# Kernel optimization log

Measured on AMD Instinct MI355X. Metric: run time of the kernel, lower is better.

Reference implementation:

```python
import jax, jax.numpy as jnp
import numpy as np

NEG_SLOPE = 0.2  # GATConv attention leaky_relu slope (init arg)
POST_SLOPE = 0.2  # leaky_relu after LayerNorm in outer forward
N_LAYERS = 3


def _leaky(x, slope):
    return jnp.where(x >= 0, x, slope * x)


def _layer_norm(x, g, b):
    mu = jnp.mean(x, axis=-1, keepdims=True)
    var = jnp.var(x, axis=-1, keepdims=True)
    return (x - mu) * jax.lax.rsqrt(var + 1e-5) * g + b


def _gat_conv(h, W, al, ar, bias, src, dst, apply_act):
    # DGL GATConv (eval mode, dropout = identity)
    N = h.shape[0]
    H, D = al.shape
    feat = (h @ W).reshape(N, H, D)                      # [N,H,D]
    el = jnp.einsum('nhd,hd->nh', feat, al)              # [N,H]
    er = jnp.einsum('nhd,hd->nh', feat, ar)              # [N,H]
    e = _leaky(el[src] + er[dst], NEG_SLOPE)             # [E,H] edge logits
    # segment (per-destination) softmax, numerically stable
    m = jax.ops.segment_max(e, dst, num_segments=N)      # [N,H]
    ex = jnp.exp(e - m[dst])                             # [E,H]
    s = jax.ops.segment_sum(ex, dst, num_segments=N)     # [N,H]
    alpha = ex / s[dst]                                  # [E,H]
    msg = alpha[:, :, None] * feat[src]                  # [E,H,D]
    rst = jax.ops.segment_sum(msg, dst, num_segments=N)  # [N,H,D]
    rst = rst + bias.reshape(1, H, D)
    if apply_act:
        rst = jax.nn.elu(rst)
    return rst


def setup_inputs() -> dict:
    key = jax.random.key(0)
    ks = jax.random.split(key, 12)
    N, E, IN, D, H, C = 100000, 1600000, 256, 64, 4, 40
    HID = H * D  # 256
    sc = 0.05
    return {
        'x': jax.random.normal(ks[0], (N, IN), jnp.float32),
        'W_h': jax.random.normal(ks[1], (3, IN, HID), jnp.float32) * sc,
        'attn_l_h': jax.random.normal(ks[2], (3, H, D), jnp.float32) * sc,
        'attn_r_h': jax.random.normal(ks[3], (3, H, D), jnp.float32) * sc,
        'bias_h': jnp.zeros((3, HID), jnp.float32),
        'ln_g': jnp.ones((3, HID), jnp.float32),
        'ln_b': jnp.zeros((3, HID), jnp.float32),
        'W_o': jax.random.normal(ks[4], (HID, C), jnp.float32) * sc,
        'attn_l_o': jax.random.normal(ks[5], (1, C), jnp.float32) * sc,
        'attn_r_o': jax.random.normal(ks[6], (1, C), jnp.float32) * sc,
        'bias_o': jnp.zeros((C,), jnp.float32),
        'edge_src': jax.random.randint(ks[7], (E,), 0, N, jnp.int32),
        'edge_dst': jax.random.randint(ks[8], (E,), 0, N, jnp.int32),
    }


def reference(x, W_h, attn_l_h, attn_r_h, bias_h, ln_g, ln_b,
              W_o, attn_l_o, attn_r_o, bias_o, edge_src, edge_dst):
    h = x
    for l in range(N_LAYERS):
        hn = _gat_conv(h, W_h[l], attn_l_h[l], attn_r_h[l], bias_h[l],
                       edge_src, edge_dst, True)
        hn = hn.reshape(hn.shape[0], -1)          # flatten heads -> [N, H*D]
        hn = _layer_norm(hn, ln_g[l], ln_b[l])
        hn = _leaky(hn, POST_SLOPE)
        h = hn + h if h.shape == hn.shape else hn  # residual when shapes match
    logits = _gat_conv(h, W_o, attn_l_o, attn_r_o, bias_o,
                       edge_src, edge_dst, False).sum(axis=1)  # sum over heads
    return logits
```

## Files before the change

### kernel.cpp

```cpp
#include <hip/hip_runtime.h>
#include <math.h>


#define NEG_SLOPE 0.2f

typedef __attribute__((ext_vector_type(8))) short bf16x8;
typedef __attribute__((ext_vector_type(4))) float floatx4;

__device__ __forceinline__ float leaky(float x) { return x >= 0.f ? x : NEG_SLOPE * x; }

__device__ __forceinline__ unsigned short f2bf(float f) {
    unsigned u = __builtin_bit_cast(unsigned, f);
    u += 0x7fffu + ((u >> 16) & 1u);
    return (unsigned short)(u >> 16);
}
__device__ __forceinline__ float bf2f(unsigned short h) {
    unsigned u = ((unsigned)h) << 16;
    return __builtin_bit_cast(float, u);
}

__global__ __launch_bounds__(256) void bucket_count(const int* __restrict__ dst,
                                                    int* __restrict__ bcnt, int E, int nbkt) {
    __shared__ int h[1024];
    for (int i = threadIdx.x; i < nbkt; i += 256) h[i] = 0;
    __syncthreads();
    const int base = blockIdx.x * 8192;
#pragma unroll 4
    for (int i = 0; i < 32; ++i) {
        int e = base + threadIdx.x + i * 256;
        if (e < E) atomicAdd(&h[dst[e] >> 7], 1);
    }
    __syncthreads();
    for (int i = threadIdx.x; i < nbkt; i += 256) {
        int v = h[i];
        if (v) atomicAdd(&bcnt[i], v);
    }
}

__global__ __launch_bounds__(256) void bucket_scan(const int* __restrict__ bcnt,
                                                   int* __restrict__ bbase,
                                                   int* __restrict__ bcursor, int nbkt) {
    __shared__ int s[256];
    const int t = threadIdx.x;
    int c[4];
    int tsum = 0;
#pragma unroll
    for (int j = 0; j < 4; ++j) {
        int i = t * 4 + j;
        c[j] = (i < nbkt) ? bcnt[i] : 0;
        tsum += c[j];
    }
    s[t] = tsum;
    __syncthreads();
    for (int off = 1; off < 256; off <<= 1) {
        int v = (t >= off) ? s[t - off] : 0;
        __syncthreads();
        s[t] += v;
        __syncthreads();
    }
    int excl = s[t] - tsum;
#pragma unroll
    for (int j = 0; j < 4; ++j) {
        int i = t * 4 + j;
        if (i < nbkt) {
            bbase[i] = excl;
            bcursor[i] = excl;
        }
        excl += c[j];
    }
}

__global__ __launch_bounds__(256) void bucket_partition(const int* __restrict__ src,
                                                        const int* __restrict__ dst,
                                                        int* __restrict__ bcursor,
                                                        int2* __restrict__ pairs, int E, int nbkt) {
    __shared__ int h[1024];
    __shared__ int basech[1024];
    for (int i = threadIdx.x; i < nbkt; i += 256) h[i] = 0;
    __syncthreads();
    const int base = blockIdx.x * 8192;
#pragma unroll 4
    for (int i = 0; i < 32; ++i) {
        int e = base + threadIdx.x + i * 256;
        if (e < E) atomicAdd(&h[dst[e] >> 7], 1);
    }
    __syncthreads();
    for (int i = threadIdx.x; i < nbkt; i += 256) {
        int v = h[i];
        basech[i] = v ? atomicAdd(&bcursor[i], v) : 0;
    }
    __syncthreads();
    for (int i = threadIdx.x; i < nbkt; i += 256) h[i] = 0;
    __syncthreads();
#pragma unroll 4
    for (int i = 0; i < 32; ++i) {
        int e = base + threadIdx.x + i * 256;
        if (e < E) {
            int d = dst[e], b = d >> 7;
            int r = atomicAdd(&h[b], 1);
            pairs[basech[b] + r] = make_int2(src[e], d);
        }
    }
}

__global__ __launch_bounds__(256) void csr_bucket(const int2* __restrict__ pairs,
                                                  const int* __restrict__ bbase,
                                                  int* __restrict__ start, int* __restrict__ endp,
                                                  int* __restrict__ col, int N, int E, int nbkt) {
    const int b = blockIdx.x;
    const int node0 = b << 7;
    int nc = N - node0;
    if (nc <= 0) return;
    if (nc > 128) nc = 128;
    __shared__ int cnt[128];
    __shared__ int s[128];
    const int t = threadIdx.x;
    if (t < 128) cnt[t] = 0;
    __syncthreads();
    const int ebase = bbase[b];
    const int eend = (b + 1 < nbkt) ? bbase[b + 1] : E;
    for (int e = ebase + t; e < eend; e += 256) {
        atomicAdd(&cnt[pairs[e].y - node0], 1);
    }
    __syncthreads();
    if (t < 128) s[t] = cnt[t];
    __syncthreads();
    for (int off = 1; off < 128; off <<= 1) {
        int v = 0;
        if (t < 128 && t >= off) v = s[t - off];
        __syncthreads();
        if (t < 128) s[t] += v;
        __syncthreads();
    }
    if (t < nc) {
        start[node0 + t] = ebase + s[t] - cnt[t];
        endp[node0 + t] = ebase + s[t];
    }
    if (t < 128) cnt[t] = s[t] - cnt[t];
    __syncthreads();
    for (int e = ebase + t; e < eend; e += 256) {
        int2 pr = pairs[e];
        int r = atomicAdd(&cnt[pr.y - node0], 1);
        col[ebase + r] = pr.x;
    }
}

__global__ void transpose_w(const float* __restrict__ W, unsigned short* __restrict__ Wt) {
    int idx = blockIdx.x * 256 + threadIdx.x;
    int l = idx >> 16, r = idx & 65535;
    int k = r >> 8, n = r & 255;
    Wt[l * 65536 + n * 256 + k] = f2bf(W[l * 65536 + k * 256 + n]);
}

__global__ void transpose_wo(const float* __restrict__ W, unsigned short* __restrict__ Wt) {
    int idx = blockIdx.x * 256 + threadIdx.x;
    int n = idx >> 8, k = idx & 255;
    Wt[n * 256 + k] = (n < 40) ? f2bf(W[k * 40 + n]) : (unsigned short)0;
}

#define BPAD 264
#define ALD 40
template <bool F32>
__global__ __launch_bounds__(512, 2) void gemm_bf16_fused(
    const void* __restrict__ Av, const unsigned short* __restrict__ Wt,
    const float* __restrict__ al, const float* __restrict__ ar,
    unsigned short* __restrict__ Cb, float* __restrict__ el, float* __restrict__ er, int M) {
    const unsigned short* Ab = (const unsigned short*)Av;
    const float* Af = (const float*)Av;
    __shared__ unsigned short Bs[256 * BPAD];
    __shared__ unsigned short As[2][128 * ALD];
    const int tid = threadIdx.x;
    const int lane = tid & 63, wid = tid >> 6;
    const int wm = (wid >> 2) * 64;
    const int wn = (wid & 3) * 64;
    const int q = lane >> 4, m = lane & 15;

#pragma unroll
    for (int i = 0; i < 16; ++i) {
        int flat = tid + 512 * i;
        int row = flat >> 5, col8 = (flat & 31) * 8;
        *(bf16x8*)&Bs[row * BPAD + col8] = *(const bf16x8*)(Wt + row * 256 + col8);
    }
    __syncthreads();

    const int rA = tid >> 2, k8 = (tid & 3) * 8;
    const int head = wid & 3;
    const float* alh = al + head * 64;
    const float* arh = ar + head * 64;
    const int c = lane & 15;
    float a0 = alh[c], a1 = alh[16 + c], a2 = alh[32 + c], a3 = alh[48 + c];
    float r0 = arh[c], r1 = arh[16 + c], r2 = arh[32 + c], r3 = arh[48 + c];

    const int ntiles = (M + 127) >> 7;
    for (int t = blockIdx.x; t < ntiles; t += gridDim.x) {
        const int row0 = t << 7;
        int agr = row0 + rA; if (agr >= M) agr = M - 1;

        auto loadA8 = [&](int kb) -> bf16x8 {
            if constexpr (F32) {
                const float* p = Af + (size_t)agr * 256 + kb + k8;
                float4 f0 = *(const float4*)p;
                float4 f1 = *(const float4*)(p + 4);
                bf16x8 v;
                v[0] = (short)f2bf(f0.x); v[1] = (short)f2bf(f0.y);
                v[2] = (short)f2bf(f0.z); v[3] = (short)f2bf(f0.w);
                v[4] = (short)f2bf(f1.x); v[5] = (short)f2bf(f1.y);
                v[6] = (short)f2bf(f1.z); v[7] = (short)f2bf(f1.w);
                return v;
            } else {
                return *(const bf16x8*)(Ab + (size_t)agr * 256 + kb + k8);
            }
        };

        bf16x8 pa = loadA8(0);
        floatx4 acc[4][4] = {};
        int cur = 0;
        for (int kb = 0; kb < 256; kb += 32) {
            *(bf16x8*)&As[cur][rA * ALD + k8] = pa;
            __syncthreads();
            if (kb + 32 < 256) pa = loadA8(kb + 32);
            bf16x8 af[4], bfr[4];
#pragma unroll
            for (int i = 0; i < 4; ++i) {
                af[i] = *(const bf16x8*)&As[cur][(wm + i * 16 + m) * ALD + q * 8];
                bfr[i] = *(const bf16x8*)&Bs[(wn + i * 16 + m) * BPAD + kb + q * 8];
            }
#pragma unroll
            for (int i = 0; i < 4; ++i)
#pragma unroll
                for (int j = 0; j < 4; ++j)
                    acc[i][j] = __builtin_amdgcn_mfma_f32_16x16x32_bf16(af[i], bfr[j], acc[i][j], 0, 0, 0);
            cur ^= 1;
        }

#pragma unroll
        for (int i = 0; i < 4; ++i)
#pragma unroll
            for (int j = 0; j < 4; ++j)
#pragma unroll
                for (int r = 0; r < 4; ++r) {
                    int grow = row0 + wm + i * 16 + q * 4 + r;
                    int gcol = wn + j * 16 + c;
                    if (grow < M) Cb[(size_t)grow * 256 + gcol] = f2bf(acc[i][j][r]);
                }

#pragma unroll
        for (int i = 0; i < 4; ++i)
#pragma unroll
            for (int r = 0; r < 4; ++r) {
                float pel = acc[i][0][r] * a0 + acc[i][1][r] * a1 + acc[i][2][r] * a2 + acc[i][3][r] * a3;
                float per = acc[i][0][r] * r0 + acc[i][1][r] * r1 + acc[i][2][r] * r2 + acc[i][3][r] * r3;
#pragma unroll
                for (int off = 8; off >= 1; off >>= 1) {
                    pel += __shfl_xor(pel, off);
                    per += __shfl_xor(per, off);
                }
                if (c == 0) {
                    int grow = row0 + wm + i * 16 + q * 4 + r;
                    if (grow < M) {
                        el[(size_t)grow * 4 + head] = pel;
                        er[(size_t)grow * 4 + head] = per;
                    }
                }
            }
        __syncthreads();
    }
}

#define LDSK 40
#define BSTRIDE 264
#define OSTR 64
__global__ __launch_bounds__(256) void gemm_out_mfma(const unsigned short* __restrict__ h,
                                                     const unsigned short* __restrict__ Wt,
                                                     const float* __restrict__ alo,
                                                     const float* __restrict__ aro,
                                                     unsigned short* __restrict__ feat_o,
                                                     float* __restrict__ elo,
                                                     float* __restrict__ ero, int N) {
    __shared__ unsigned short As[128 * LDSK];
    __shared__ unsigned short Bs[48 * BSTRIDE];
    const int tid = threadIdx.x;
    const int row0 = blockIdx.x * 128;
    const int lane = tid & 63, wid = tid >> 6;

#pragma unroll
    for (int i = 0; i < 6; ++i) {
        int f = tid + 256 * i;
        int n = f >> 5, kk = (f & 31) * 8;
        *(bf16x8*)&Bs[n * BSTRIDE + kk] = *(const bf16x8*)(Wt + n * 256 + kk);
    }
    __syncthreads();

    floatx4 acc[2][3] = {};
    for (int kb = 0; kb < 256; kb += 32) {
#pragma unroll
        for (int i = 0; i < 2; ++i) {
            int idx = tid + 256 * i;
            int r = idx >> 2, k8 = (idx & 3) * 8;
            int gr = row0 + r;
            bf16x8 v = {};
            if (gr < N) v = *(const bf16x8*)(h + (size_t)gr * 256 + kb + k8);
            *(bf16x8*)&As[r * LDSK + k8] = v;
        }
        __syncthreads();
        const int q = lane >> 4, m = lane & 15;
        bf16x8 af[2], bfr[3];
#pragma unroll
        for (int i = 0; i < 2; ++i)
            af[i] = *(const bf16x8*)&As[(wid * 32 + i * 16 + m) * LDSK + q * 8];
#pragma unroll
        for (int j = 0; j < 3; ++j)
            bfr[j] = *(const bf16x8*)&Bs[(j * 16 + m) * BSTRIDE + kb + q * 8];
#pragma unroll
        for (int i = 0; i < 2; ++i)
#pragma unroll
            for (int j = 0; j < 3; ++j)
                acc[i][j] = __builtin_amdgcn_mfma_f32_16x16x32_bf16(af[i], bfr[j], acc[i][j], 0, 0, 0);
        __syncthreads();
    }

    const int q = lane >> 4, c = lane & 15;
#pragma unroll
    for (int i = 0; i < 2; ++i)
#pragma unroll
        for (int j = 0; j < 3; ++j)
#pragma unroll
            for (int r = 0; r < 4; ++r) {
                int grow = row0 + wid * 32 + i * 16 + q * 4 + r;
                int gcol = j * 16 + c;
                if (grow < N && gcol < 40) feat_o[(size_t)grow * OSTR + gcol] = f2bf(acc[i][j][r]);
            }

    float aj[3], rj[3];
#pragma unroll
    for (int j = 0; j < 3; ++j) {
        int gcol = j * 16 + c;
        aj[j] = gcol < 40 ? alo[gcol] : 0.f;
        rj[j] = gcol < 40 ? aro[gcol] : 0.f;
    }
#pragma unroll
    for (int i = 0; i < 2; ++i)
#pragma unroll
        for (int r = 0; r < 4; ++r) {
            float pl = acc[i][0][r] * aj[0] + acc[i][1][r] * aj[1] + acc[i][2][r] * aj[2];
            float pr = acc[i][0][r] * rj[0] + acc[i][1][r] * rj[1] + acc[i][2][r] * rj[2];
#pragma unroll
            for (int off = 8; off >= 1; off >>= 1) {
                pl += __shfl_xor(pl, off);
                pr += __shfl_xor(pr, off);
            }
            if (c == 0) {
                int grow = row0 + wid * 32 + i * 16 + q * 4 + r;
                if (grow < N) {
                    elo[grow] = pl;
                    ero[grow] = pr;
                }
            }
        }
}

__global__ __launch_bounds__(256) void aggregate_hidden(
    const unsigned short* __restrict__ feat, const float* __restrict__ el,
    const float* __restrict__ er, const int* __restrict__ start, const int* __restrict__ endp,
    const int* __restrict__ col, const float* __restrict__ bias, const float* __restrict__ lng,
    const float* __restrict__ lnb, const unsigned short* __restrict__ h_in,
    const float* __restrict__ h_in_f32,
    unsigned short* __restrict__ h_out, int node0, int nend) {
    int node = node0 + blockIdx.x * 4 + (threadIdx.x >> 6);
    int lane = threadIdx.x & 63;
    if (node >= nend) return;
    int begin = __builtin_amdgcn_readfirstlane(start[node]);
    int end = __builtin_amdgcn_readfirstlane(endp[node]);
    const int head = lane >> 4;
    const float erh = er[(size_t)node * 4 + head];

    const int ch = lane * 4;
    const unsigned short* fbase = feat + ch;
    const size_t hstr = 256;
    float4 acc = {0.f, 0.f, 0.f, 0.f};
    float ssum = 0.f;
    int e = begin;
    for (; e + 7 < end; e += 8) {
        int sA = col[e], sB = col[e + 1], sC = col[e + 2], sD = col[e + 3];
        int sE = col[e + 4], sF = col[e + 5], sG = col[e + 6], sH = col[e + 7];
        float eA = el[(size_t)sA * 4 + head];
        float eB = el[(size_t)sB * 4 + head];
        float eC = el[(size_t)sC * 4 + head];
        float eD = el[(size_t)sD * 4 + head];
        float eE = el[(size_t)sE * 4 + head];
        float eF = el[(size_t)sF * 4 + head];
        float eG = el[(size_t)sG * 4 + head];
        float eH = el[(size_t)sH * 4 + head];
        ushort4 uA = *(const ushort4*)(fbase + sA * hstr);
        ushort4 uB = *(const ushort4*)(fbase + sB * hstr);
        ushort4 uC = *(const ushort4*)(fbase + sC * hstr);
        ushort4 uD = *(const ushort4*)(fbase + sD * hstr);
        ushort4 uE = *(const ushort4*)(fbase + sE * hstr);
        ushort4 uF = *(const ushort4*)(fbase + sF * hstr);
        ushort4 uG = *(const ushort4*)(fbase + sG * hstr);
        ushort4 uH = *(const ushort4*)(fbase + sH * hstr);
        float wA = __expf(leaky(eA + erh));
        float wB = __expf(leaky(eB + erh));
        float wC = __expf(leaky(eC + erh));
        float wD = __expf(leaky(eD + erh));
        float wE = __expf(leaky(eE + erh));
        float wF = __expf(leaky(eF + erh));
        float wG = __expf(leaky(eG + erh));
        float wH = __expf(leaky(eH + erh));
        ssum += wA + wB + wC + wD + wE + wF + wG + wH;
        acc.x = fmaf(wA, bf2f(uA.x), acc.x); acc.y = fmaf(wA, bf2f(uA.y), acc.y);
        acc.z = fmaf(wA, bf2f(uA.z), acc.z); acc.w = fmaf(wA, bf2f(uA.w), acc.w);
        acc.x = fmaf(wB, bf2f(uB.x), acc.x); acc.y = fmaf(wB, bf2f(uB.y), acc.y);
        acc.z = fmaf(wB, bf2f(uB.z), acc.z); acc.w = fmaf(wB, bf2f(uB.w), acc.w);
        acc.x = fmaf(wC, bf2f(uC.x), acc.x); acc.y = fmaf(wC, bf2f(uC.y), acc.y);
        acc.z = fmaf(wC, bf2f(uC.z), acc.z); acc.w = fmaf(wC, bf2f(uC.w), acc.w);
        acc.x = fmaf(wD, bf2f(uD.x), acc.x); acc.y = fmaf(wD, bf2f(uD.y), acc.y);
        acc.z = fmaf(wD, bf2f(uD.z), acc.z); acc.w = fmaf(wD, bf2f(uD.w), acc.w);
        acc.x = fmaf(wE, bf2f(uE.x), acc.x); acc.y = fmaf(wE, bf2f(uE.y), acc.y);
        acc.z = fmaf(wE, bf2f(uE.z), acc.z); acc.w = fmaf(wE, bf2f(uE.w), acc.w);
        acc.x = fmaf(wF, bf2f(uF.x), acc.x); acc.y = fmaf(wF, bf2f(uF.y), acc.y);
        acc.z = fmaf(wF, bf2f(uF.z), acc.z); acc.w = fmaf(wF, bf2f(uF.w), acc.w);
        acc.x = fmaf(wG, bf2f(uG.x), acc.x); acc.y = fmaf(wG, bf2f(uG.y), acc.y);
        acc.z = fmaf(wG, bf2f(uG.z), acc.z); acc.w = fmaf(wG, bf2f(uG.w), acc.w);
        acc.x = fmaf(wH, bf2f(uH.x), acc.x); acc.y = fmaf(wH, bf2f(uH.y), acc.y);
        acc.z = fmaf(wH, bf2f(uH.z), acc.z); acc.w = fmaf(wH, bf2f(uH.w), acc.w);
    }
    for (; e < end; ++e) {
        int sA = col[e];
        float wA = __expf(leaky(el[(size_t)sA * 4 + head] + erh));
        ushort4 uA = *(const ushort4*)(fbase + sA * hstr);
        ssum += wA;
        acc.x = fmaf(wA, bf2f(uA.x), acc.x); acc.y = fmaf(wA, bf2f(uA.y), acc.y);
        acc.z = fmaf(wA, bf2f(uA.z), acc.z); acc.w = fmaf(wA, bf2f(uA.w), acc.w);
    }
    float inv = ssum > 0.f ? 1.f / ssum : 0.f;
    acc.x *= inv; acc.y *= inv; acc.z *= inv; acc.w *= inv;

    float4 bb = *(const float4*)(bias + ch);
    float x0 = acc.x + bb.x, x1 = acc.y + bb.y, x2 = acc.z + bb.z, x3 = acc.w + bb.w;
    x0 = x0 > 0.f ? x0 : expm1f(x0);
    x1 = x1 > 0.f ? x1 : expm1f(x1);
    x2 = x2 > 0.f ? x2 : expm1f(x2);
    x3 = x3 > 0.f ? x3 : expm1f(x3);
    float lsum = x0 + x1 + x2 + x3;
    float lsq = x0 * x0 + x1 * x1 + x2 * x2 + x3 * x3;
#pragma unroll
    for (int off = 32; off >= 1; off >>= 1) {
        lsum += __shfl_xor(lsum, off);
        lsq += __shfl_xor(lsq, off);
    }
    float mu = lsum * (1.f / 256.f);
    float var = lsq * (1.f / 256.f) - mu * mu;
    float rstd = rsqrtf(var + 1e-5f);
    float4 g4 = *(const float4*)(lng + ch);
    float4 b4 = *(const float4*)(lnb + ch);
    float rx, ry, rz, rw;
    if (h_in_f32) {
        float4 hf = *(const float4*)(h_in_f32 + (size_t)node * 256 + ch);
        rx = hf.x; ry = hf.y; rz = hf.z; rw = hf.w;
    } else {
        ushort4 hi = *(const ushort4*)(h_in + (size_t)node * 256 + ch);
        rx = bf2f(hi.x); ry = bf2f(hi.y); rz = bf2f(hi.z); rw = bf2f(hi.w);
    }
    float y0 = (x0 - mu) * rstd * g4.x + b4.x;
    float y1 = (x1 - mu) * rstd * g4.y + b4.y;
    float y2 = (x2 - mu) * rstd * g4.z + b4.z;
    float y3 = (x3 - mu) * rstd * g4.w + b4.w;
    y0 = (y0 >= 0.f ? y0 : 0.2f * y0) + rx;
    y1 = (y1 >= 0.f ? y1 : 0.2f * y1) + ry;
    y2 = (y2 >= 0.f ? y2 : 0.2f * y2) + rz;
    y3 = (y3 >= 0.f ? y3 : 0.2f * y3) + rw;
    ushort4 o;
    o.x = f2bf(y0); o.y = f2bf(y1); o.z = f2bf(y2); o.w = f2bf(y3);
    *(ushort4*)(h_out + (size_t)node * 256 + ch) = o;
}

__global__ __launch_bounds__(256) void aggregate_out(const unsigned short* __restrict__ feat_o,
                                                     const float* __restrict__ elo,
                                                     const float* __restrict__ ero,
                                                     const int* __restrict__ start,
                                                     const int* __restrict__ endp,
                                                     const int* __restrict__ col,
                                                     const float* __restrict__ bias_o,
                                                     float* __restrict__ out, int node0, int nend) {
    int node = node0 + blockIdx.x * 4 + (threadIdx.x >> 6);
    int lane = threadIdx.x & 63;
    if (node >= nend) return;
    int begin = __builtin_amdgcn_readfirstlane(start[node]);
    int end = __builtin_amdgcn_readfirstlane(endp[node]);
    float ern = ero[node];
    int cc = lane < 40 ? lane : 0;
    float acc = 0.f, ssum = 0.f;
    int e = begin;
    for (; e + 7 < end; e += 8) {
        int sA = col[e], sB = col[e + 1], sC = col[e + 2], sD = col[e + 3];
        int sE = col[e + 4], sF = col[e + 5], sG = col[e + 6], sH = col[e + 7];
        float eA = elo[sA], eB = elo[sB], eC = elo[sC], eD = elo[sD];
        float eE = elo[sE], eF = elo[sF], eG = elo[sG], eH = elo[sH];
        unsigned short fA = feat_o[(size_t)sA * OSTR + cc];
        unsigned short fB = feat_o[(size_t)sB * OSTR + cc];
        unsigned short fC = feat_o[(size_t)sC * OSTR + cc];
        unsigned short fD = feat_o[(size_t)sD * OSTR + cc];
        unsigned short fE = feat_o[(size_t)sE * OSTR + cc];
        unsigned short fF = feat_o[(size_t)sF * OSTR + cc];
        unsigned short fG = feat_o[(size_t)sG * OSTR + cc];
        unsigned short fH = feat_o[(size_t)sH * OSTR + cc];
        float wA = __expf(leaky(eA + ern));
        float wB = __expf(leaky(eB + ern));
        float wC = __expf(leaky(eC + ern));
        float wD = __expf(leaky(eD + ern));
        float wE = __expf(leaky(eE + ern));
        float wF = __expf(leaky(eF + ern));
        float wG = __expf(leaky(eG + ern));
        float wH = __expf(leaky(eH + ern));
        ssum += wA + wB + wC + wD + wE + wF + wG + wH;
        acc = fmaf(wA, bf2f(fA), acc);
        acc = fmaf(wB, bf2f(fB), acc);
        acc = fmaf(wC, bf2f(fC), acc);
        acc = fmaf(wD, bf2f(fD), acc);
        acc = fmaf(wE, bf2f(fE), acc);
        acc = fmaf(wF, bf2f(fF), acc);
        acc = fmaf(wG, bf2f(fG), acc);
        acc = fmaf(wH, bf2f(fH), acc);
    }
    for (; e < end; ++e) {
        int sA = col[e];
        float wA = __expf(leaky(elo[sA] + ern));
        ssum += wA;
        acc = fmaf(wA, bf2f(feat_o[(size_t)sA * OSTR + cc]), acc);
    }
    float inv = ssum > 0.f ? 1.f / ssum : 0.f;
    if (lane < 40) out[(size_t)node * 40 + lane] = acc * inv + bias_o[lane];
}

extern "C" void kernel_launch(void* const* d_in, const int* in_sizes, int n_in,
                              void* d_out, int out_size, void* d_ws, size_t ws_size,
                              hipStream_t stream) {
    const float* x = (const float*)d_in[0];
    const float* W_h = (const float*)d_in[1];
    const float* al_h = (const float*)d_in[2];
    const float* ar_h = (const float*)d_in[3];
    const float* bias_h = (const float*)d_in[4];
    const float* ln_g = (const float*)d_in[5];
    const float* ln_b = (const float*)d_in[6];
    const float* W_o = (const float*)d_in[7];
    const float* al_o = (const float*)d_in[8];
    const float* ar_o = (const float*)d_in[9];
    const float* bias_o = (const float*)d_in[10];
    const int* esrc = (const int*)d_in[11];
    const int* edst = (const int*)d_in[12];
    const int N = in_sizes[0] / 256;
    const int E = in_sizes[11];
    float* out = (float*)d_out;

    char* ws = (char*)d_ws;
    size_t off = 0;
    auto walloc = [&](size_t bytes) -> void* {
        void* p = ws + off;
        off += (bytes + 255) & ~(size_t)255;
        return p;
    };
    unsigned short* h_bf = (unsigned short*)walloc((size_t)N * 256 * 2);
    unsigned short* feat_bf = (unsigned short*)walloc((size_t)N * 256 * 2);
    unsigned short* Wt = (unsigned short*)walloc((size_t)3 * 65536 * 2);
    unsigned short* Wt_o = (unsigned short*)walloc((size_t)48 * 256 * 2);
    float* el = (float*)walloc((size_t)N * 4 * 4);
    float* er = (float*)walloc((size_t)N * 4 * 4);
    int* start = (int*)walloc((size_t)N * 4);
    int* endp = (int*)walloc((size_t)N * 4);
    int* col = (int*)walloc((size_t)E * 4);
    int* bcnt = (int*)walloc(1024 * 4);
    int* bbase = (int*)walloc(1024 * 4);
    int* bcursor = (int*)walloc(1024 * 4);
    int2* pairs = (int2*)walloc((size_t)E * 8);
    if (off > ws_size) return;

    const int TB = 256;
    const int nbkt = (N + 127) >> 7;
    const int nbe = (E + 8191) / 8192;
    transpose_w<<<3 * 65536 / TB, TB, 0, stream>>>(W_h, Wt);
    transpose_wo<<<48, TB, 0, stream>>>(W_o, Wt_o);
    hipMemsetAsync(bcnt, 0, (size_t)nbkt * 4, stream);
    bucket_count<<<nbe, TB, 0, stream>>>(edst, bcnt, E, nbkt);
    bucket_scan<<<1, TB, 0, stream>>>(bcnt, bbase, bcursor, nbkt);
    bucket_partition<<<nbe, TB, 0, stream>>>(esrc, edst, bcursor, pairs, E, nbkt);
    csr_bucket<<<nbkt, TB, 0, stream>>>(pairs, bbase, start, endp, col, N, E, nbkt);

    const int N2 = ((N / 2) + 3) & ~3;
    const int nbh1 = (N2 + 3) / 4;
    const int nbh2 = (N - N2 + 3) / 4;
    for (int l = 0; l < 3; ++l) {
        if (l == 0) {
            gemm_bf16_fused<true><<<256, 512, 0, stream>>>(x, Wt,
                                                           al_h, ar_h,
                                                           feat_bf, el, er, N);
        } else {
            gemm_bf16_fused<false><<<256, 512, 0, stream>>>(h_bf, Wt + (size_t)l * 65536,
                                                            al_h + l * 256, ar_h + l * 256,
                                                            feat_bf, el, er, N);
        }
        const unsigned short* hin_bf = h_bf;
        const float* hin_f32 = (l == 0) ? x : nullptr;
        aggregate_hidden<<<nbh1, 256, 0, stream>>>(feat_bf, el, er, start, endp, col,
                                                   bias_h + l * 256, ln_g + l * 256,
                                                   ln_b + l * 256, hin_bf, hin_f32, h_bf, 0, N2);
        aggregate_hidden<<<nbh2, 256, 0, stream>>>(feat_bf, el, er, start, endp, col,
                                                   bias_h + l * 256, ln_g + l * 256,
                                                   ln_b + l * 256, hin_bf, hin_f32, h_bf, N2, N);
    }
    unsigned short* feat_o = feat_bf;
    float* elo = el;
    float* ero = er;
    gemm_out_mfma<<<(N + 127) / 128, 256, 0, stream>>>(h_bf, Wt_o, al_o, ar_o, feat_o, elo, ero, N);
    aggregate_out<<<nbh1, 256, 0, stream>>>(feat_o, elo, ero, start, endp, col, bias_o, out, 0, N2);
    aggregate_out<<<nbh2, 256, 0, stream>>>(feat_o, elo, ero, start, endp, col, bias_o, out, N2, N);
}
```

Measured before the change: 908.6 us.

## Drop LDS staging in GEMMs; load MFMA fragments directly from global memory

Both the hidden-layer GEMM and the output GEMM stop staging A and B tiles in shared memory. Each wave now loads its MFMA operand fragments straight from global memory (L2/L1), which removes the barriers and LDS traffic. The hidden GEMM also moves from a persistent 256-block, 512-thread launch with the full weight matrix in LDS to a non-persistent grid of 128x128 tiles with two column blocks per row tile. This trades LDS reuse for more redundant global and cache reads of A and W, and loses the explicit prefetch double-buffering.

```diff
diff --git a/kernel.cpp b/kernel.cpp
--- a/kernel.cpp
+++ b/kernel.cpp
@@ -158,47 +158,44 @@
     Wt[n * 256 + k] = (n < 40) ? f2bf(W[k * 40 + n]) : (unsigned short)0;
 }
 
-#define BPAD 264
-#define ALD 40
 template <bool F32>
-__global__ __launch_bounds__(512, 2) void gemm_bf16_fused(
+__global__ __launch_bounds__(256) void gemm_fused(
     const void* __restrict__ Av, const unsigned short* __restrict__ Wt,
     const float* __restrict__ al, const float* __restrict__ ar,
     unsigned short* __restrict__ Cb, float* __restrict__ el, float* __restrict__ er, int M) {
     const unsigned short* Ab = (const unsigned short*)Av;
     const float* Af = (const float*)Av;
-    __shared__ unsigned short Bs[256 * BPAD];
-    __shared__ unsigned short As[2][128 * ALD];
     const int tid = threadIdx.x;
     const int lane = tid & 63, wid = tid >> 6;
-    const int wm = (wid >> 2) * 64;
-    const int wn = (wid & 3) * 64;
+    const int bx = blockIdx.x & 1;
+    const int by = blockIdx.x >> 1;
+    const int row0 = by * 128, col0 = bx * 128;
+    const int wm = (wid >> 1) * 64;
+    const int wn = (wid & 1) * 64;
     const int q = lane >> 4, m = lane & 15;
 
-#pragma unroll
-    for (int i = 0; i < 16; ++i) {
-        int flat = tid + 512 * i;
-        int row = flat >> 5, col8 = (flat & 31) * 8;
-        *(bf16x8*)&Bs[row * BPAD + col8] = *(const bf16x8*)(Wt + row * 256 + col8);
-    }
-    __syncthreads();
-
-    const int rA = tid >> 2, k8 = (tid & 3) * 8;
-    const int head = wid & 3;
-    const float* alh = al + head * 64;
-    const float* arh = ar + head * 64;
-    const int c = lane & 15;
-    float a0 = alh[c], a1 = alh[16 + c], a2 = alh[32 + c], a3 = alh[48 + c];
-    float r0 = arh[c], r1 = arh[16 + c], r2 = arh[32 + c], r3 = arh[48 + c];
-
-    const int ntiles = (M + 127) >> 7;
-    for (int t = blockIdx.x; t < ntiles; t += gridDim.x) {
-        const int row0 = t << 7;
-        int agr = row0 + rA; if (agr >= M) agr = M - 1;
-
-        auto loadA8 = [&](int kb) -> bf16x8 {
+    const unsigned short* ap[4];
+    const float* apf[4];
+    const unsigned short* bp[4];
+#pragma unroll
+    for (int i = 0; i < 4; ++i) {
+        int r = row0 + wm + i * 16 + m;
+        if (r >= M) r = M - 1;
+        ap[i] = Ab + (size_t)r * 256 + q * 8;
+        apf[i] = Af + (size_t)r * 256 + q * 8;
+        bp[i] = Wt + (size_t)(col0 + wn + i * 16 + m) * 256 + q * 8;
+    }
+
+    floatx4 acc[4][4] = {};
+#pragma unroll 2
+    for (int kb = 0; kb < 256; kb += 32) {
+        bf16x8 af[4], bfr[4];
+#pragma unroll
+        for (int i = 0; i < 4; ++i) bfr[i] = *(const bf16x8*)(bp[i] + kb);
+#pragma unroll
+        for (int i = 0; i < 4; ++i) {
             if constexpr (F32) {
-                const float* p = Af + (size_t)agr * 256 + kb + k8;
+                const float* p = apf[i] + kb;
                 float4 f0 = *(const float4*)p;
                 float4 f1 = *(const float4*)(p + 4);
                 bf16x8 v;
@@ -206,69 +203,56 @@
                 v[2] = (short)f2bf(f0.z); v[3] = (short)f2bf(f0.w);
                 v[4] = (short)f2bf(f1.x); v[5] = (short)f2bf(f1.y);
                 v[6] = (short)f2bf(f1.z); v[7] = (short)f2bf(f1.w);
-                return v;
+                af[i] = v;
             } else {
-                return *(const bf16x8*)(Ab + (size_t)agr * 256 + kb + k8);
-            }
-        };
-
-        bf16x8 pa = loadA8(0);
-        floatx4 acc[4][4] = {};
-        int cur = 0;
-        for (int kb = 0; kb < 256; kb += 32) {
-            *(bf16x8*)&As[cur][rA * ALD + k8] = pa;
-            __syncthreads();
-            if (kb + 32 < 256) pa = loadA8(kb + 32);
-            bf16x8 af[4], bfr[4];
-#pragma unroll
-            for (int i = 0; i < 4; ++i) {
-                af[i] = *(const bf16x8*)&As[cur][(wm + i * 16 + m) * ALD + q * 8];
-                bfr[i] = *(const bf16x8*)&Bs[(wn + i * 16 + m) * BPAD + kb + q * 8];
-            }
-#pragma unroll
-            for (int i = 0; i < 4; ++i)
-#pragma unroll
-                for (int j = 0; j < 4; ++j)
-                    acc[i][j] = __builtin_amdgcn_mfma_f32_16x16x32_bf16(af[i], bfr[j], acc[i][j], 0, 0, 0);
-            cur ^= 1;
+                af[i] = *(const bf16x8*)(ap[i] + kb);
+            }
         }
-
 #pragma unroll
         for (int i = 0; i < 4; ++i)
 #pragma unroll
             for (int j = 0; j < 4; ++j)
-#pragma unroll
-                for (int r = 0; r < 4; ++r) {
-                    int grow = row0 + wm + i * 16 + q * 4 + r;
-                    int gcol = wn + j * 16 + c;
-                    if (grow < M) Cb[(size_t)grow * 256 + gcol] = f2bf(acc[i][j][r]);
+                acc[i][j] = __builtin_amdgcn_mfma_f32_16x16x32_bf16(af[i], bfr[j], acc[i][j], 0, 0, 0);
+    }
+
+    const int c = lane & 15;
+#pragma unroll
+    for (int i = 0; i < 4; ++i)
+#pragma unroll
+        for (int j = 0; j < 4; ++j)
+#pragma unroll
+            for (int r = 0; r < 4; ++r) {
+                int grow = row0 + wm + i * 16 + q * 4 + r;
+                int gcol = col0 + wn + j * 16 + c;
+                if (grow < M) Cb[(size_t)grow * 256 + gcol] = f2bf(acc[i][j][r]);
+            }
+
+    const int head = bx * 2 + (wn >> 6);
+    const float* alh = al + head * 64;
+    const float* arh = ar + head * 64;
+    float a0 = alh[c], a1 = alh[16 + c], a2 = alh[32 + c], a3 = alh[48 + c];
+    float r0 = arh[c], r1 = arh[16 + c], r2 = arh[32 + c], r3 = arh[48 + c];
+#pragma unroll
+    for (int i = 0; i < 4; ++i)
+#pragma unroll
+        for (int r = 0; r < 4; ++r) {
+            float pel = acc[i][0][r] * a0 + acc[i][1][r] * a1 + acc[i][2][r] * a2 + acc[i][3][r] * a3;
+            float per = acc[i][0][r] * r0 + acc[i][1][r] * r1 + acc[i][2][r] * r2 + acc[i][3][r] * r3;
+#pragma unroll
+            for (int off = 8; off >= 1; off >>= 1) {
+                pel += __shfl_xor(pel, off);
+                per += __shfl_xor(per, off);
+            }
+            if (c == 0) {
+                int grow = row0 + wm + i * 16 + q * 4 + r;
+                if (grow < M) {
+                    el[(size_t)grow * 4 + head] = pel;
+                    er[(size_t)grow * 4 + head] = per;
                 }
-
-#pragma unroll
-        for (int i = 0; i < 4; ++i)
-#pragma unroll
-            for (int r = 0; r < 4; ++r) {
-                float pel = acc[i][0][r] * a0 + acc[i][1][r] * a1 + acc[i][2][r] * a2 + acc[i][3][r] * a3;
-                float per = acc[i][0][r] * r0 + acc[i][1][r] * r1 + acc[i][2][r] * r2 + acc[i][3][r] * r3;
-#pragma unroll
-                for (int off = 8; off >= 1; off >>= 1) {
-                    pel += __shfl_xor(pel, off);
-                    per += __shfl_xor(per, off);
-                }
-                if (c == 0) {
-                    int grow = row0 + wm + i * 16 + q * 4 + r;
-                    if (grow < M) {
-                        el[(size_t)grow * 4 + head] = pel;
-                        er[(size_t)grow * 4 + head] = per;
-                    }
-                }
-            }
-        __syncthreads();
-    }
-}
-
-#define LDSK 40
-#define BSTRIDE 264
+            }
+        }
+}
+
 #define OSTR 64
 __global__ __launch_bounds__(256) void gemm_out_mfma(const unsigned short* __restrict__ h,
                                                      const unsigned short* __restrict__ Wt,
@@ -277,49 +261,38 @@
                                                      unsigned short* __restrict__ feat_o,
                                                      float* __restrict__ elo,
                                                      float* __restrict__ ero, int N) {
-    __shared__ unsigned short As[128 * LDSK];
-    __shared__ unsigned short Bs[48 * BSTRIDE];
     const int tid = threadIdx.x;
     const int row0 = blockIdx.x * 128;
     const int lane = tid & 63, wid = tid >> 6;
-
-#pragma unroll
-    for (int i = 0; i < 6; ++i) {
-        int f = tid + 256 * i;
-        int n = f >> 5, kk = (f & 31) * 8;
-        *(bf16x8*)&Bs[n * BSTRIDE + kk] = *(const bf16x8*)(Wt + n * 256 + kk);
-    }
-    __syncthreads();
+    const int q = lane >> 4, m = lane & 15;
+
+    const unsigned short* ap[2];
+    const unsigned short* bp[3];
+#pragma unroll
+    for (int i = 0; i < 2; ++i) {
+        int r = row0 + wid * 32 + i * 16 + m;
+        if (r >= N) r = N - 1;
+        ap[i] = h + (size_t)r * 256 + q * 8;
+    }
+#pragma unroll
+    for (int j = 0; j < 3; ++j) bp[j] = Wt + (size_t)(j * 16 + m) * 256 + q * 8;
 
     floatx4 acc[2][3] = {};
+#pragma unroll 2
     for (int kb = 0; kb < 256; kb += 32) {
-#pragma unroll
-        for (int i = 0; i < 2; ++i) {
-            int idx = tid + 256 * i;
-            int r = idx >> 2, k8 = (idx & 3) * 8;
-            int gr = row0 + r;
-            bf16x8 v = {};
-            if (gr < N) v = *(const bf16x8*)(h + (size_t)gr * 256 + kb + k8);
-            *(bf16x8*)&As[r * LDSK + k8] = v;
-        }
-        __syncthreads();
-        const int q = lane >> 4, m = lane & 15;
         bf16x8 af[2], bfr[3];
 #pragma unroll
-        for (int i = 0; i < 2; ++i)
-            af[i] = *(const bf16x8*)&As[(wid * 32 + i * 16 + m) * LDSK + q * 8];
-#pragma unroll
-        for (int j = 0; j < 3; ++j)
-            bfr[j] = *(const bf16x8*)&Bs[(j * 16 + m) * BSTRIDE + kb + q * 8];
+        for (int i = 0; i < 2; ++i) af[i] = *(const bf16x8*)(ap[i] + kb);
+#pragma unroll
+        for (int j = 0; j < 3; ++j) bfr[j] = *(const bf16x8*)(bp[j] + kb);
 #pragma unroll
         for (int i = 0; i < 2; ++i)
 #pragma unroll
             for (int j = 0; j < 3; ++j)
                 acc[i][j] = __builtin_amdgcn_mfma_f32_16x16x32_bf16(af[i], bfr[j], acc[i][j], 0, 0, 0);
-        __syncthreads();
-    }
-
-    const int q = lane >> 4, c = lane & 15;
+    }
+
+    const int c = lane & 15;
 #pragma unroll
     for (int i = 0; i < 2; ++i)
 #pragma unroll
@@ -589,15 +562,15 @@
     const int N2 = ((N / 2) + 3) & ~3;
     const int nbh1 = (N2 + 3) / 4;
     const int nbh2 = (N - N2 + 3) / 4;
+    const int gemm_grid = ((N + 127) / 128) * 2;
     for (int l = 0; l < 3; ++l) {
         if (l == 0) {
-            gemm_bf16_fused<true><<<256, 512, 0, stream>>>(x, Wt,
-                                                           al_h, ar_h,
-                                                           feat_bf, el, er, N);
+            gemm_fused<true><<<gemm_grid, 256, 0, stream>>>(x, Wt, al_h, ar_h,
+                                                            feat_bf, el, er, N);
         } else {
-            gemm_bf16_fused<false><<<256, 512, 0, stream>>>(h_bf, Wt + (size_t)l * 65536,
-                                                            al_h + l * 256, ar_h + l * 256,
-                                                            feat_bf, el, er, N);
+            gemm_fused<false><<<gemm_grid, 256, 0, stream>>>(h_bf, Wt + (size_t)l * 65536,
+                                                             al_h + l * 256, ar_h + l * 256,
+                                                             feat_bf, el, er, N);
         }
         const unsigned short* hin_bf = h_bf;
         const float* hin_f32 = (l == 0) ? x : nullptr;
```

New measurement: 1.004 ms. 1.1x slower.

## Stream W tiles via global_load_lds and stage GEMM output through LDS

Applied to the files above, without the earlier changes.

The hidden-layer GEMM stops keeping the whole 256x256 weight matrix resident in LDS. It now double-buffers 32-wide K slices of both A and W, loading them with direct global-to-LDS copies, which cuts LDS use enough to raise occupancy to 4 blocks per CU. The persistent 256-block grid becomes one block per 128-row tile. The epilogue transposes accumulators through LDS so output rows are written as coalesced 8-byte vectors instead of scattered 2-byte stores. In exchange, W is re-read from global/L2 by every tile. The unpadded 32-element LDS rows may also cause bank conflicts on the fragment reads.

```diff
diff --git a/kernel.cpp b/kernel.cpp
--- a/kernel.cpp
+++ b/kernel.cpp
@@ -17,6 +17,12 @@
 __device__ __forceinline__ float bf2f(unsigned short h) {
     unsigned u = ((unsigned)h) << 16;
     return __builtin_bit_cast(float, u);
+}
+
+typedef const __attribute__((address_space(1))) unsigned int* as1_u32p;
+typedef __attribute__((address_space(3))) unsigned int* as3_u32p;
+__device__ __forceinline__ void gl_lds16(const void* g, void* l) {
+    __builtin_amdgcn_global_load_lds((as1_u32p)g, (as3_u32p)l, 16, 0, 0);
 }
 
 __global__ __launch_bounds__(256) void bucket_count(const int* __restrict__ dst,
@@ -158,113 +164,115 @@
     Wt[n * 256 + k] = (n < 40) ? f2bf(W[k * 40 + n]) : (unsigned short)0;
 }
 
-#define BPAD 264
-#define ALD 40
 template <bool F32>
-__global__ __launch_bounds__(512, 2) void gemm_bf16_fused(
+__global__ __launch_bounds__(512, 4) void gemm_fused(
     const void* __restrict__ Av, const unsigned short* __restrict__ Wt,
     const float* __restrict__ al, const float* __restrict__ ar,
     unsigned short* __restrict__ Cb, float* __restrict__ el, float* __restrict__ er, int M) {
     const unsigned short* Ab = (const unsigned short*)Av;
     const float* Af = (const float*)Av;
-    __shared__ unsigned short Bs[256 * BPAD];
-    __shared__ unsigned short As[2][128 * ALD];
+    __shared__ unsigned short SMEM[24576];
+    unsigned short* As = SMEM;
+    unsigned short* Bs = SMEM + 2 * 128 * 32;
     const int tid = threadIdx.x;
+    const int row0 = blockIdx.x * 128;
     const int lane = tid & 63, wid = tid >> 6;
     const int wm = (wid >> 2) * 64;
     const int wn = (wid & 3) * 64;
     const int q = lane >> 4, m = lane & 15;
 
-#pragma unroll
-    for (int i = 0; i < 16; ++i) {
-        int flat = tid + 512 * i;
-        int row = flat >> 5, col8 = (flat & 31) * 8;
-        *(bf16x8*)&Bs[row * BPAD + col8] = *(const bf16x8*)(Wt + row * 256 + col8);
-    }
-    __syncthreads();
-
-    const int rA = tid >> 2, k8 = (tid & 3) * 8;
+    const int arow = wid * 16 + (lane >> 2);
+    const int brow0 = wid * 32 + (lane >> 2);
+    const int kx = (lane & 3) * 8;
+    const int agr = (row0 + arow < M) ? (row0 + arow) : (M - 1);
+
+    auto stage = [&](int buf, int kb) {
+        if constexpr (F32) {
+            const float* p = Af + (size_t)agr * 256 + kb + kx;
+            float4 f0 = *(const float4*)p;
+            float4 f1 = *(const float4*)(p + 4);
+            bf16x8 v;
+            v[0] = (short)f2bf(f0.x); v[1] = (short)f2bf(f0.y);
+            v[2] = (short)f2bf(f0.z); v[3] = (short)f2bf(f0.w);
+            v[4] = (short)f2bf(f1.x); v[5] = (short)f2bf(f1.y);
+            v[6] = (short)f2bf(f1.z); v[7] = (short)f2bf(f1.w);
+            *(bf16x8*)&As[buf * 128 * 32 + arow * 32 + kx] = v;
+        } else {
+            gl_lds16(Ab + (size_t)agr * 256 + kb + kx, &As[buf * 128 * 32 + arow * 32 + kx]);
+        }
+        gl_lds16(Wt + (size_t)brow0 * 256 + kb + kx, &Bs[buf * 256 * 32 + brow0 * 32 + kx]);
+        gl_lds16(Wt + (size_t)(brow0 + 16) * 256 + kb + kx,
+                 &Bs[buf * 256 * 32 + (brow0 + 16) * 32 + kx]);
+    };
+
+    floatx4 acc[4][4] = {};
+    stage(0, 0);
+    __syncthreads();
+    int cur = 0;
+    for (int kb = 0; kb < 256; kb += 32) {
+        int nkb = kb + 32;
+        if (nkb < 256) stage(cur ^ 1, nkb);
+        bf16x8 af[4], bfr[4];
+#pragma unroll
+        for (int i = 0; i < 4; ++i) {
+            af[i] = *(const bf16x8*)&As[cur * 128 * 32 + (wm + i * 16 + m) * 32 + q * 8];
+            bfr[i] = *(const bf16x8*)&Bs[cur * 256 * 32 + (wn + i * 16 + m) * 32 + q * 8];
+        }
+#pragma unroll
+        for (int i = 0; i < 4; ++i)
+#pragma unroll
+            for (int j = 0; j < 4; ++j)
+                acc[i][j] = __builtin_amdgcn_mfma_f32_16x16x32_bf16(af[i], bfr[j], acc[i][j], 0, 0, 0);
+        __syncthreads();
+        cur ^= 1;
+    }
+    float* rep = (float*)SMEM + wid * 1088;
+    const int c = lane & 15;
+#pragma unroll
+    for (int i = 0; i < 4; ++i) {
+#pragma unroll
+        for (int j = 0; j < 4; ++j)
+#pragma unroll
+            for (int r = 0; r < 4; ++r)
+                rep[(q * 4 + r) * 68 + j * 16 + c] = acc[i][j][r];
+#pragma unroll
+        for (int p = 0; p < 4; ++p) {
+            int row16 = p * 4 + (lane >> 4);
+            int c4 = (lane & 15) * 4;
+            float4 v = *(const float4*)&rep[row16 * 68 + c4];
+            int grow = row0 + wm + i * 16 + row16;
+            if (grow < M) {
+                ushort4 o;
+                o.x = f2bf(v.x); o.y = f2bf(v.y); o.z = f2bf(v.z); o.w = f2bf(v.w);
+                *(ushort4*)(Cb + (size_t)grow * 256 + wn + c4) = o;
+            }
+        }
+    }
+
     const int head = wid & 3;
     const float* alh = al + head * 64;
     const float* arh = ar + head * 64;
-    const int c = lane & 15;
     float a0 = alh[c], a1 = alh[16 + c], a2 = alh[32 + c], a3 = alh[48 + c];
     float r0 = arh[c], r1 = arh[16 + c], r2 = arh[32 + c], r3 = arh[48 + c];
-
-    const int ntiles = (M + 127) >> 7;
-    for (int t = blockIdx.x; t < ntiles; t += gridDim.x) {
-        const int row0 = t << 7;
-        int agr = row0 + rA; if (agr >= M) agr = M - 1;
-
-        auto loadA8 = [&](int kb) -> bf16x8 {
-            if constexpr (F32) {
-                const float* p = Af + (size_t)agr * 256 + kb + k8;
-                float4 f0 = *(const float4*)p;
-                float4 f1 = *(const float4*)(p + 4);
-                bf16x8 v;
-                v[0] = (short)f2bf(f0.x); v[1] = (short)f2bf(f0.y);
-                v[2] = (short)f2bf(f0.z); v[3] = (short)f2bf(f0.w);
-                v[4] = (short)f2bf(f1.x); v[5] = (short)f2bf(f1.y);
-                v[6] = (short)f2bf(f1.z); v[7] = (short)f2bf(f1.w);
-                return v;
-            } else {
-                return *(const bf16x8*)(Ab + (size_t)agr * 256 + kb + k8);
+#pragma unroll
+    for (int i = 0; i < 4; ++i)
+#pragma unroll
+        for (int r = 0; r < 4; ++r) {
+            float pel = acc[i][0][r] * a0 + acc[i][1][r] * a1 + acc[i][2][r] * a2 + acc[i][3][r] * a3;
+            float per = acc[i][0][r] * r0 + acc[i][1][r] * r1 + acc[i][2][r] * r2 + acc[i][3][r] * r3;
+#pragma unroll
+            for (int off = 8; off >= 1; off >>= 1) {
+                pel += __shfl_xor(pel, off);
+                per += __shfl_xor(per, off);
             }
-        };
-
-        bf16x8 pa = loadA8(0);
-        floatx4 acc[4][4] = {};
-        int cur = 0;
-        for (int kb = 0; kb < 256; kb += 32) {
-            *(bf16x8*)&As[cur][rA * ALD + k8] = pa;
-            __syncthreads();
-            if (kb + 32 < 256) pa = loadA8(kb + 32);
-            bf16x8 af[4], bfr[4];
-#pragma unroll
-            for (int i = 0; i < 4; ++i) {
-                af[i] = *(const bf16x8*)&As[cur][(wm + i * 16 + m) * ALD + q * 8];
-                bfr[i] = *(const bf16x8*)&Bs[(wn + i * 16 + m) * BPAD + kb + q * 8];
-            }
-#pragma unroll
-            for (int i = 0; i < 4; ++i)
-#pragma unroll
-                for (int j = 0; j < 4; ++j)
-                    acc[i][j] = __builtin_amdgcn_mfma_f32_16x16x32_bf16(af[i], bfr[j], acc[i][j], 0, 0, 0);
-            cur ^= 1;
-        }
-
-#pragma unroll
-        for (int i = 0; i < 4; ++i)
-#pragma unroll
-            for (int j = 0; j < 4; ++j)
-#pragma unroll
-                for (int r = 0; r < 4; ++r) {
-                    int grow = row0 + wm + i * 16 + q * 4 + r;
-                    int gcol = wn + j * 16 + c;
-                    if (grow < M) Cb[(size_t)grow * 256 + gcol] = f2bf(acc[i][j][r]);
-                }
-
-#pragma unroll
-        for (int i = 0; i < 4; ++i)
-#pragma unroll
-            for (int r = 0; r < 4; ++r) {
-                float pel = acc[i][0][r] * a0 + acc[i][1][r] * a1 + acc[i][2][r] * a2 + acc[i][3][r] * a3;
-                float per = acc[i][0][r] * r0 + acc[i][1][r] * r1 + acc[i][2][r] * r2 + acc[i][3][r] * r3;
-#pragma unroll
-                for (int off = 8; off >= 1; off >>= 1) {
-                    pel += __shfl_xor(pel, off);
-                    per += __shfl_xor(per, off);
-                }
-                if (c == 0) {
-                    int grow = row0 + wm + i * 16 + q * 4 + r;
-                    if (grow < M) {
-                        el[(size_t)grow * 4 + head] = pel;
-                        er[(size_t)grow * 4 + head] = per;
-                    }
+            if (c == 0) {
+                int grow = row0 + wm + i * 16 + q * 4 + r;
+                if (grow < M) {
+                    el[(size_t)grow * 4 + head] = pel;
+                    er[(size_t)grow * 4 + head] = per;
                 }
             }
-        __syncthreads();
-    }
+        }
 }
 
 #define LDSK 40
@@ -589,15 +597,15 @@
     const int N2 = ((N / 2) + 3) & ~3;
     const int nbh1 = (N2 + 3) / 4;
     const int nbh2 = (N - N2 + 3) / 4;
+    const int gemm_grid = (N + 127) / 128;
     for (int l = 0; l < 3; ++l) {
         if (l == 0) {
-            gemm_bf16_fused<true><<<256, 512, 0, stream>>>(x, Wt,
-                                                           al_h, ar_h,
-                                                           feat_bf, el, er, N);
+            gemm_fused<true><<<gemm_grid, 512, 0, stream>>>(x, Wt, al_h, ar_h,
+                                                            feat_bf, el, er, N);
         } else {
-            gemm_bf16_fused<false><<<256, 512, 0, stream>>>(h_bf, Wt + (size_t)l * 65536,
-                                                            al_h + l * 256, ar_h + l * 256,
-                                                            feat_bf, el, er, N);
+            gemm_fused<false><<<gemm_grid, 512, 0, stream>>>(h_bf, Wt + (size_t)l * 65536,
+                                                             al_h + l * 256, ar_h + l * 256,
+                                                             feat_bf, el, er, N);
         }
         const unsigned short* hin_bf = h_bf;
         const float* hin_f32 = (l == 0) ? x : nullptr;
```

New measurement: 871.8 us. -4.1%, faster.
